# Kernel optimization log

Measured on AMD Instinct MI355X. Metric: run time of the kernel, lower is better.

The kernel has to match this reference:

```python
import jax, jax.numpy as jnp
import numpy as np

HEADS = 16

def split_heads(v, heads):
    # NOTE: faithful to the source: reshape [B,S,D] -> [B,S,h_dim,heads], then
    # transpose to [B,heads,S,h_dim]. This interleaves channels across heads
    # (different from the standard [B,S,heads,h_dim] split).
    B, S, D = v.shape
    hd = D // heads
    return v.reshape(B, S, hd, heads).transpose(0, 3, 1, 2)

def merge_heads(v):
    # [B,heads,S,h_dim] -> transpose [B,S,h_dim,heads] -> reshape [B,S,D]
    B, H, S, hd = v.shape
    return v.transpose(0, 2, 3, 1).reshape(B, S, H * hd)

def setup_inputs() -> dict:
    key = jax.random.key(0)
    ks = jax.random.split(key, 5)
    B, S, D = 2, 2048, 1024
    return {
        "x": jax.random.normal(ks[0], (B, S, D), dtype=jnp.float32),
        "qw": jax.random.normal(ks[1], (D, D), dtype=jnp.float32),
        "kw": jax.random.normal(ks[2], (D, D), dtype=jnp.float32),
        "vw": jax.random.normal(ks[3], (D, D), dtype=jnp.float32),
        "ow": jax.random.normal(ks[4], (D, D), dtype=jnp.float32),
    }

def reference(x, qw, kw, vw, ow):
    B, S, D = x.shape
    Q = split_heads(x @ qw, HEADS)  # [B,H,S,hd]
    K = split_heads(x @ kw, HEADS)
    V = split_heads(x @ vw, HEADS)
    # NOTE: scale is 1/sqrt(dim), NOT 1/sqrt(head_dim), as in the source.
    scale = 1.0 / jnp.sqrt(jnp.float32(D))
    score = jnp.einsum("bhqd,bhkd->bhqk", Q, K) * scale  # [B,H,S,S]
    causal = jnp.tril(jnp.ones((1, 1, S, S), dtype=score.dtype))
    score = score - 1e10 * (1.0 - causal)
    weights = jax.nn.softmax(score, axis=-1)
    attn = jnp.einsum("bhqk,bhkd->bhqd", weights, V)
    return merge_heads(attn) @ ow
```

## Files before the change

### kernel.cpp

```cpp
#include <hip/hip_runtime.h>


typedef __bf16 bf16x8 __attribute__((ext_vector_type(8)));
typedef __bf16 bf16x4 __attribute__((ext_vector_type(4)));
typedef float  f32x4  __attribute__((ext_vector_type(4)));

#define S_LEN  2048
#define DMODEL 1024
#define NHEADS 16
#define HDIM   64
#define LOG2E  1.44269504088896340736f

__device__ __forceinline__ void gll16(const __bf16* g, __bf16* l) {
    __builtin_amdgcn_global_load_lds(
        (const __attribute__((address_space(1))) unsigned int*)g,
        (__attribute__((address_space(3))) unsigned int*)l, 16, 0, 0);
}

__global__ __launch_bounds__(256) void conv_split(const float* __restrict__ x,
                                                  __bf16* __restrict__ hi,
                                                  __bf16* __restrict__ lo, int n4) {
    int i = blockIdx.x * 256 + threadIdx.x;
    if (i >= n4) return;
    float4 v = ((const float4*)x)[i];
    bf16x4 h, l;
#pragma unroll
    for (int c = 0; c < 4; c++) {
        float f = (&v.x)[c];
        __bf16 fh = (__bf16)f;
        h[c] = fh;
        l[c] = (__bf16)(f - (float)fh);
    }
    ((bf16x4*)hi)[i] = h;
    ((bf16x4*)lo)[i] = l;
}

__global__ __launch_bounds__(256) void transpose_all(
    const float* __restrict__ qw, const float* __restrict__ kw,
    const float* __restrict__ vw, const float* __restrict__ ow,
    __bf16* __restrict__ qwthi, __bf16* __restrict__ qwtlo,
    __bf16* __restrict__ kwthi, __bf16* __restrict__ kwtlo,
    __bf16* __restrict__ vwt,  __bf16* __restrict__ owt) {
    __shared__ float tile[32][33];
    int z = blockIdx.z;
    const float* w = (z == 0) ? qw : (z == 1) ? kw : (z == 2) ? vw : ow;
    int n0 = blockIdx.x * 32, k0 = blockIdx.y * 32;
    int tx = threadIdx.x & 31, ty = threadIdx.x >> 5;
#pragma unroll
    for (int i = 0; i < 32; i += 8)
        tile[ty + i][tx] = w[(k0 + ty + i) * DMODEL + n0 + tx];
    __syncthreads();
#pragma unroll
    for (int i = 0; i < 32; i += 8) {
        float f = tile[tx][ty + i];
        int k = k0 + tx, n = n0 + ty + i;
        if (z <= 1) {
            __bf16 fh = (__bf16)f;
            __bf16 fl = (__bf16)(f - (float)fh);
            int c = (n & 15) * 64 + (n >> 4);
            if (z == 0) { qwthi[c * DMODEL + k] = fh; qwtlo[c * DMODEL + k] = fl; }
            else        { kwthi[c * DMODEL + k] = fh; kwtlo[c * DMODEL + k] = fl; }
        } else if (z == 2) {
            vwt[n * DMODEL + k] = (__bf16)f;
        } else {
            int ck = (k & 15) * 64 + (k >> 4);
            owt[n * DMODEL + ck] = (__bf16)f;
        }
    }
}

__global__ __launch_bounds__(256) void qkv_gemm(
    const __bf16* __restrict__ xhi, const __bf16* __restrict__ xlo,
    const __bf16* __restrict__ qwthi, const __bf16* __restrict__ qwtlo,
    const __bf16* __restrict__ kwthi, const __bf16* __restrict__ kwtlo,
    const __bf16* __restrict__ vwt,
    __bf16* __restrict__ Qhi, __bf16* __restrict__ Qlo,
    __bf16* __restrict__ Khi, __bf16* __restrict__ Klo,
    __bf16* __restrict__ Vt) {
    __shared__ __bf16 Ash[128][32], Asl[128][32], Bsh[128][32], Bsl[128][32];
    int mode = blockIdx.z;
    int tid  = threadIdx.x;
    int wave = tid >> 6, lane = tid & 63;
    int quad = lane >> 4, l15 = lane & 15;
    int wm = (wave >> 1) * 64, wn = (wave & 1) * 64;
    int grow = lane >> 2, gcol = (lane & 3) * 8;
    const int K = DMODEL;

    if (mode < 2) {
        const __bf16* Bh = mode ? kwthi : qwthi;
        const __bf16* Bl = mode ? kwtlo : qwtlo;
        int m0 = blockIdx.y * 128, n0 = blockIdx.x * 128;
        f32x4 acc[4][4] = {};
        for (int k0 = 0; k0 < K; k0 += 32) {
            __syncthreads();
#pragma unroll
            for (int ps = 0; ps < 2; ps++) {
                int row = ps * 64 + wave * 16;
                gll16(&xhi[(m0 + row + grow) * K + k0 + gcol], &Ash[row][0]);
                gll16(&xlo[(m0 + row + grow) * K + k0 + gcol], &Asl[row][0]);
                gll16(&Bh [(n0 + row + grow) * K + k0 + gcol], &Bsh[row][0]);
                gll16(&Bl [(n0 + row + grow) * K + k0 + gcol], &Bsl[row][0]);
            }
            __syncthreads();
            bf16x8 ah[4], al[4], bh[4], bl[4];
#pragma unroll
            for (int mi = 0; mi < 4; mi++) {
                ah[mi] = *(const bf16x8*)&Ash[wm + mi * 16 + l15][quad * 8];
                al[mi] = *(const bf16x8*)&Asl[wm + mi * 16 + l15][quad * 8];
            }
#pragma unroll
            for (int ni = 0; ni < 4; ni++) {
                bh[ni] = *(const bf16x8*)&Bsh[wn + ni * 16 + l15][quad * 8];
                bl[ni] = *(const bf16x8*)&Bsl[wn + ni * 16 + l15][quad * 8];
            }
#pragma unroll
            for (int mi = 0; mi < 4; mi++)
#pragma unroll
                for (int ni = 0; ni < 4; ni++) {
                    acc[mi][ni] = __builtin_amdgcn_mfma_f32_16x16x32_bf16(ah[mi], bh[ni], acc[mi][ni], 0, 0, 0);
                    acc[mi][ni] = __builtin_amdgcn_mfma_f32_16x16x32_bf16(ah[mi], bl[ni], acc[mi][ni], 0, 0, 0);
                    acc[mi][ni] = __builtin_amdgcn_mfma_f32_16x16x32_bf16(al[mi], bh[ni], acc[mi][ni], 0, 0, 0);
                }
        }
        float oscale = mode ? 1.0f : 0.03125f * LOG2E;
        __bf16* Ohi = mode ? Khi : Qhi;
        __bf16* Olo = mode ? Klo : Qlo;
#pragma unroll
        for (int mi = 0; mi < 4; mi++)
#pragma unroll
            for (int ni = 0; ni < 4; ni++)
#pragma unroll
                for (int rg = 0; rg < 4; rg++) {
                    int m = m0 + wm + mi * 16 + quad * 4 + rg;
                    int n = n0 + wn + ni * 16 + l15;
                    float v = acc[mi][ni][rg] * oscale;
                    size_t idx = (size_t)m * DMODEL + n;
                    __bf16 vh = (__bf16)v;
                    Ohi[idx] = vh;
                    Olo[idx] = (__bf16)(v - (float)vh);
                }
    } else {
        int ch0 = blockIdx.x * 128, xm0 = blockIdx.y * 128;
        f32x4 acc[4][4] = {};
        for (int k0 = 0; k0 < K; k0 += 32) {
            __syncthreads();
#pragma unroll
            for (int ps = 0; ps < 2; ps++) {
                int row = ps * 64 + wave * 16;
                gll16(&vwt[(ch0 + row + grow) * K + k0 + gcol], &Ash[row][0]);
                gll16(&xhi[(xm0 + row + grow) * K + k0 + gcol], &Bsh[row][0]);
            }
            __syncthreads();
            bf16x8 af[4], bfr[4];
#pragma unroll
            for (int mi = 0; mi < 4; mi++)
                af[mi] = *(const bf16x8*)&Ash[wm + mi * 16 + l15][quad * 8];
#pragma unroll
            for (int ni = 0; ni < 4; ni++)
                bfr[ni] = *(const bf16x8*)&Bsh[wn + ni * 16 + l15][quad * 8];
#pragma unroll
            for (int mi = 0; mi < 4; mi++)
#pragma unroll
                for (int ni = 0; ni < 4; ni++)
                    acc[mi][ni] = __builtin_amdgcn_mfma_f32_16x16x32_bf16(
                        af[mi], bfr[ni], acc[mi][ni], 0, 0, 0);
        }
#pragma unroll
        for (int mi = 0; mi < 4; mi++)
#pragma unroll
            for (int ni = 0; ni < 4; ni++)
#pragma unroll
                for (int rg = 0; rg < 4; rg++) {
                    int ch = ch0 + wm + mi * 16 + quad * 4 + rg;
                    int xm = xm0 + wn + ni * 16 + l15;
                    int b = xm >> 11, s = xm & 2047;
                    int h = ch & 15,  d = ch >> 4;
                    Vt[((size_t)(b * NHEADS + h) * HDIM + d) * S_LEN + s] =
                        (__bf16)acc[mi][ni][rg];
                }
    }
}

__global__ __launch_bounds__(256) void out_gemm(const __bf16* __restrict__ A,
                                                const __bf16* __restrict__ Bt,
                                                float* __restrict__ out) {
    __shared__ __bf16 As[64][32];
    __shared__ __bf16 Bs[128][32];
    int tid  = threadIdx.x;
    int wave = tid >> 6, lane = tid & 63;
    int quad = lane >> 4, l15 = lane & 15;
    int m0 = blockIdx.y * 64, n0 = blockIdx.x * 128;
    int wm = (wave >> 1) * 32, wn = (wave & 1) * 64;
    int grow = lane >> 2, gcol = (lane & 3) * 8;
    const int K = DMODEL;
    f32x4 acc[2][4] = {};

    for (int k0 = 0; k0 < K; k0 += 32) {
        __syncthreads();
        gll16(&A[(m0 + wave * 16 + grow) * K + k0 + gcol], &As[wave * 16][0]);
#pragma unroll
        for (int ps = 0; ps < 2; ps++) {
            int row = ps * 64 + wave * 16;
            gll16(&Bt[(n0 + row + grow) * K + k0 + gcol], &Bs[row][0]);
        }
        __syncthreads();
        bf16x8 af[2], bfr[4];
#pragma unroll
        for (int mi = 0; mi < 2; mi++)
            af[mi] = *(const bf16x8*)&As[wm + mi * 16 + l15][quad * 8];
#pragma unroll
        for (int ni = 0; ni < 4; ni++)
            bfr[ni] = *(const bf16x8*)&Bs[wn + ni * 16 + l15][quad * 8];
#pragma unroll
        for (int mi = 0; mi < 2; mi++)
#pragma unroll
            for (int ni = 0; ni < 4; ni++)
                acc[mi][ni] = __builtin_amdgcn_mfma_f32_16x16x32_bf16(
                    af[mi], bfr[ni], acc[mi][ni], 0, 0, 0);
    }

#pragma unroll
    for (int mi = 0; mi < 2; mi++)
#pragma unroll
        for (int ni = 0; ni < 4; ni++)
#pragma unroll
            for (int rg = 0; rg < 4; rg++) {
                int m = m0 + wm + mi * 16 + quad * 4 + rg;
                int n = n0 + wn + ni * 16 + l15;
                out[(size_t)m * DMODEL + n] = acc[mi][ni][rg];
            }
}

__global__ __launch_bounds__(256, 4) void flash_attn(const __bf16* __restrict__ Qhi,
                                                     const __bf16* __restrict__ Qlo,
                                                     const __bf16* __restrict__ Khi,
                                                     const __bf16* __restrict__ Klo,
                                                     const __bf16* __restrict__ Vt,
                                                     __bf16* __restrict__ attn) {
    int id = blockIdx.x;
    int xcd = id & 7, which = id >> 3;
    int bh  = xcd + 8 * (which & 3);
    int p   = which >> 2;
    int b = bh >> 4, h = bh & 15;
    const __bf16* Qh_hi = Qhi + (size_t)b * S_LEN * DMODEL + h * HDIM;
    const __bf16* Qh_lo = Qlo + (size_t)b * S_LEN * DMODEL + h * HDIM;
    const __bf16* Kh_hi = Khi + (size_t)b * S_LEN * DMODEL + h * HDIM;
    const __bf16* Kh_lo = Klo + (size_t)b * S_LEN * DMODEL + h * HDIM;
    const __bf16* Vh    = Vt  + (size_t)bh * HDIM * S_LEN;

    int tid = threadIdx.x, wave = tid >> 6, lane = tid & 63;
    int quad = lane >> 4, l15 = lane & 15;
    int t1 = p, t2 = 31 - p;
    int n1 = t1 + 1;

    __shared__ __bf16 KhF[8 * 64 * 8];
    __shared__ __bf16 KlF[8 * 64 * 8];
    __shared__ __bf16 VF [8 * 64 * 8];
    __shared__ __bf16 Ps[4][16][72];

    int c1  = tid >> 6, key = tid & 63;
    int inner = (c1 * 16 + (key & 15)) * 8;
    int rK    = (key >> 4);
    int kdst0 = rK * 512 + inner, kdst1 = (4 + rK) * 512 + inner;
    const __bf16* vrow = Vh + (size_t)key * S_LEN;

    int q0w = t1 * 64 + wave * 16;
    bf16x8 aqh0 = *(const bf16x8*)&Qh_hi[(size_t)(q0w + l15) * DMODEL + quad * 8];
    bf16x8 aqh1 = *(const bf16x8*)&Qh_hi[(size_t)(q0w + l15) * DMODEL + 32 + quad * 8];
    bf16x8 aql0 = *(const bf16x8*)&Qh_lo[(size_t)(q0w + l15) * DMODEL + quad * 8];
    bf16x8 aql1 = *(const bf16x8*)&Qh_lo[(size_t)(q0w + l15) * DMODEL + 32 + quad * 8];

    bf16x8 ones;
#pragma unroll
    for (int j = 0; j < 8; j++) ones[j] = (__bf16)1.0f;

    uint4 pk0, pk1, pl0, pl1, pv0, pv1;
    {
        const __bf16* sk = Kh_hi + (size_t)key * DMODEL;
        const __bf16* sl = Kh_lo + (size_t)key * DMODEL;
        pk0 = *(const uint4*)(sk + c1 * 8); pk1 = *(const uint4*)(sk + c1 * 8 + 32);
        pl0 = *(const uint4*)(sl + c1 * 8); pl1 = *(const uint4*)(sl + c1 * 8 + 32);
        pv0 = *(const uint4*)(vrow + c1 * 8); pv1 = *(const uint4*)(vrow + c1 * 8 + 32);
    }

    float m[4] = {-3e38f, -3e38f, -3e38f, -3e38f};
    f32x4 o[4] = {};
    f32x4 ol = {};
    int qrb = q0w + quad * 4;

    for (int i = 0; i < 33; i++) {
        int kt   = (i < n1) ? i : i - n1;
        int key0 = kt * 64;
        bool diag = (i == n1 - 1) || (i == 32);

        __syncthreads();
        *(uint4*)&KhF[kdst0] = pk0;  *(uint4*)&KhF[kdst1] = pk1;
        *(uint4*)&KlF[kdst0] = pl0;  *(uint4*)&KlF[kdst1] = pl1;
        *(uint4*)&VF [kdst0] = pv0;  *(uint4*)&VF [kdst1] = pv1;
        __syncthreads();

        if (i + 1 < 33) {
            int ktn   = (i + 1 < n1) ? i + 1 : i + 1 - n1;
            int key0n = ktn * 64;
            const __bf16* sk = Kh_hi + (size_t)(key0n + key) * DMODEL;
            const __bf16* sl = Kh_lo + (size_t)(key0n + key) * DMODEL;
            pk0 = *(const uint4*)(sk + c1 * 8); pk1 = *(const uint4*)(sk + c1 * 8 + 32);
            pl0 = *(const uint4*)(sl + c1 * 8); pl1 = *(const uint4*)(sl + c1 * 8 + 32);
            pv0 = *(const uint4*)(vrow + key0n + c1 * 8);
            pv1 = *(const uint4*)(vrow + key0n + c1 * 8 + 32);
        }

        f32x4 sc[4] = {};
#pragma unroll
        for (int ni = 0; ni < 4; ni++) {
            bf16x8 kh0 = *(const bf16x8*)&KhF[(ni * 64 + lane) * 8];
            bf16x8 kh1 = *(const bf16x8*)&KhF[((4 + ni) * 64 + lane) * 8];
            bf16x8 kl0 = *(const bf16x8*)&KlF[(ni * 64 + lane) * 8];
            bf16x8 kl1 = *(const bf16x8*)&KlF[((4 + ni) * 64 + lane) * 8];
            sc[ni] = __builtin_amdgcn_mfma_f32_16x16x32_bf16(aqh0, kh0, sc[ni], 0, 0, 0);
            sc[ni] = __builtin_amdgcn_mfma_f32_16x16x32_bf16(aqh1, kh1, sc[ni], 0, 0, 0);
            sc[ni] = __builtin_amdgcn_mfma_f32_16x16x32_bf16(aqh0, kl0, sc[ni], 0, 0, 0);
            sc[ni] = __builtin_amdgcn_mfma_f32_16x16x32_bf16(aqh1, kl1, sc[ni], 0, 0, 0);
            sc[ni] = __builtin_amdgcn_mfma_f32_16x16x32_bf16(aql0, kh0, sc[ni], 0, 0, 0);
            sc[ni] = __builtin_amdgcn_mfma_f32_16x16x32_bf16(aql1, kh1, sc[ni], 0, 0, 0);
        }

        if (diag) {
#pragma unroll
            for (int ni = 0; ni < 4; ni++) {
                int keyi = key0 + ni * 16 + l15;
#pragma unroll
                for (int rg = 0; rg < 4; rg++)
                    if (keyi > qrb + rg) sc[ni][rg] = -1e30f;
            }
        }

#pragma unroll
        for (int rg = 0; rg < 4; rg++) {
            float mx = fmaxf(fmaxf(sc[0][rg], sc[1][rg]),
                             fmaxf(sc[2][rg], sc[3][rg]));
#pragma unroll
            for (int mm = 1; mm < 16; mm <<= 1)
                mx = fmaxf(mx, __shfl_xor(mx, mm, 64));
            float mnew  = fmaxf(m[rg], mx);
            float alpha = __builtin_amdgcn_exp2f(m[rg] - mnew);
            m[rg] = mnew;
#pragma unroll
            for (int ni = 0; ni < 4; ni++) {
                float px = __builtin_amdgcn_exp2f(sc[ni][rg] - mnew);
                Ps[wave][quad * 4 + rg][ni * 16 + l15] = (__bf16)px;
            }
            ol[rg] *= alpha;
#pragma unroll
            for (int ni = 0; ni < 4; ni++)
                o[ni][rg] *= alpha;
        }

#pragma unroll
        for (int step = 0; step < 2; step++) {
            bf16x8 ap = *(const bf16x8*)&Ps[wave][l15][step * 32 + quad * 8];
            ol = __builtin_amdgcn_mfma_f32_16x16x32_bf16(ap, ones, ol, 0, 0, 0);
#pragma unroll
            for (int ni = 0; ni < 4; ni++) {
                bf16x8 bv = *(const bf16x8*)&VF[((step * 4 + ni) * 64 + lane) * 8];
                o[ni] = __builtin_amdgcn_mfma_f32_16x16x32_bf16(ap, bv, o[ni], 0, 0, 0);
            }
        }

        if (diag) {
#pragma unroll
            for (int rg = 0; rg < 4; rg++) {
                float inv = 1.0f / ol[rg];
                int q = q0w + quad * 4 + rg;
#pragma unroll
                for (int ni = 0; ni < 4; ni++) {
                    attn[((size_t)b * S_LEN + q) * DMODEL + h * HDIM + ni * 16 + l15] =
                        (__bf16)(o[ni][rg] * inv);
                }
                m[rg] = -3e38f;
            }
#pragma unroll
            for (int ni = 0; ni < 4; ni++) o[ni] = (f32x4){0.f, 0.f, 0.f, 0.f};
            ol = (f32x4){0.f, 0.f, 0.f, 0.f};
            if (i == n1 - 1) {
                q0w = t2 * 64 + wave * 16;
                qrb = q0w + quad * 4;
                aqh0 = *(const bf16x8*)&Qh_hi[(size_t)(q0w + l15) * DMODEL + quad * 8];
                aqh1 = *(const bf16x8*)&Qh_hi[(size_t)(q0w + l15) * DMODEL + 32 + quad * 8];
                aql0 = *(const bf16x8*)&Qh_lo[(size_t)(q0w + l15) * DMODEL + quad * 8];
                aql1 = *(const bf16x8*)&Qh_lo[(size_t)(q0w + l15) * DMODEL + 32 + quad * 8];
            }
        }
    }
}

extern "C" void kernel_launch(void* const* d_in, const int* in_sizes, int n_in,
                              void* d_out, int out_size, void* d_ws, size_t ws_size,
                              hipStream_t stream) {
    const float* x  = (const float*)d_in[0];
    const float* qw = (const float*)d_in[1];
    const float* kw = (const float*)d_in[2];
    const float* vw = (const float*)d_in[3];
    const float* ow = (const float*)d_in[4];

    char* ws = (char*)d_ws;
    const size_t MB = 1024 * 1024;
    __bf16* xhi   = (__bf16*)(ws);
    __bf16* xlo   = (__bf16*)(ws + 8 * MB);
    __bf16* qwthi = (__bf16*)(ws + 16 * MB);
    __bf16* qwtlo = (__bf16*)(ws + 18 * MB);
    __bf16* kwthi = (__bf16*)(ws + 20 * MB);
    __bf16* kwtlo = (__bf16*)(ws + 22 * MB);
    __bf16* vwt   = (__bf16*)(ws + 24 * MB);
    __bf16* owt   = (__bf16*)(ws + 26 * MB);
    __bf16* Qhi_b = (__bf16*)(ws + 28 * MB);
    __bf16* Qlo_b = (__bf16*)(ws + 36 * MB);
    __bf16* Khi_b = (__bf16*)(ws + 44 * MB);
    __bf16* Klo_b = (__bf16*)(ws + 52 * MB);
    __bf16* Vtb   = (__bf16*)(ws + 60 * MB);
    __bf16* attnb = xlo;

    conv_split<<<4096, 256, 0, stream>>>(x, xhi, xlo, 4096 * 1024 / 4);
    transpose_all<<<dim3(32, 32, 4), 256, 0, stream>>>(
        qw, kw, vw, ow, qwthi, qwtlo, kwthi, kwtlo, vwt, owt);

    qkv_gemm<<<dim3(8, 32, 3), 256, 0, stream>>>(
        xhi, xlo, qwthi, qwtlo, kwthi, kwtlo, vwt,
        Qhi_b, Qlo_b, Khi_b, Klo_b, Vtb);

    flash_attn<<<512, 256, 0, stream>>>(Qhi_b, Qlo_b, Khi_b, Klo_b, Vtb, attnb);

    out_gemm<<<dim3(8, 64), 256, 0, stream>>>(attnb, owt, (float*)d_out);
}
```

Baseline: 254.5 us.

## Split paired causal query tiles into separate blocks, longest-first scheduling

The flash attention kernel no longer pairs query tile p with tile 31-p inside one block. It launches 1024 blocks, one per query tile, ordered so the longest tiles (most key tiles) are dispatched first and the hardware scheduler balances the rest. This doubles parallelism and simplifies the loop and epilogue, but each block now loads its Q and pays its own startup. The input split kernel is also rewritten to use scalar bit casts and ushort4 stores.

```diff
diff --git a/kernel.cpp b/kernel.cpp
--- a/kernel.cpp
+++ b/kernel.cpp
@@ -2,7 +2,6 @@
 
 
 typedef __bf16 bf16x8 __attribute__((ext_vector_type(8)));
-typedef __bf16 bf16x4 __attribute__((ext_vector_type(4)));
 typedef float  f32x4  __attribute__((ext_vector_type(4)));
 
 #define S_LEN  2048
@@ -23,16 +22,20 @@
     int i = blockIdx.x * 256 + threadIdx.x;
     if (i >= n4) return;
     float4 v = ((const float4*)x)[i];
-    bf16x4 h, l;
-#pragma unroll
-    for (int c = 0; c < 4; c++) {
-        float f = (&v.x)[c];
-        __bf16 fh = (__bf16)f;
-        h[c] = fh;
-        l[c] = (__bf16)(f - (float)fh);
-    }
-    ((bf16x4*)hi)[i] = h;
-    ((bf16x4*)lo)[i] = l;
+    __bf16 h0 = (__bf16)v.x, h1 = (__bf16)v.y, h2 = (__bf16)v.z, h3 = (__bf16)v.w;
+    bf16x8 dummy;
+    (void)dummy;
+    ushort4 hh, ll;
+    hh.x = __builtin_bit_cast(unsigned short, h0);
+    hh.y = __builtin_bit_cast(unsigned short, h1);
+    hh.z = __builtin_bit_cast(unsigned short, h2);
+    hh.w = __builtin_bit_cast(unsigned short, h3);
+    ll.x = __builtin_bit_cast(unsigned short, (__bf16)(v.x - (float)h0));
+    ll.y = __builtin_bit_cast(unsigned short, (__bf16)(v.y - (float)h1));
+    ll.z = __builtin_bit_cast(unsigned short, (__bf16)(v.z - (float)h2));
+    ll.w = __builtin_bit_cast(unsigned short, (__bf16)(v.w - (float)h3));
+    ((ushort4*)hi)[i] = hh;
+    ((ushort4*)lo)[i] = ll;
 }
 
 __global__ __launch_bounds__(256) void transpose_all(
@@ -237,10 +240,10 @@
                                                      const __bf16* __restrict__ Klo,
                                                      const __bf16* __restrict__ Vt,
                                                      __bf16* __restrict__ attn) {
-    int id = blockIdx.x;
-    int xcd = id & 7, which = id >> 3;
-    int bh  = xcd + 8 * (which & 3);
-    int p   = which >> 2;
+    int id  = blockIdx.x;
+    int xcd = id & 7, r = id >> 3;
+    int bh  = xcd + 8 * (r & 3);
+    int t   = 31 - (r >> 2);
     int b = bh >> 4, h = bh & 15;
     const __bf16* Qh_hi = Qhi + (size_t)b * S_LEN * DMODEL + h * HDIM;
     const __bf16* Qh_lo = Qlo + (size_t)b * S_LEN * DMODEL + h * HDIM;
@@ -250,8 +253,7 @@
 
     int tid = threadIdx.x, wave = tid >> 6, lane = tid & 63;
     int quad = lane >> 4, l15 = lane & 15;
-    int t1 = p, t2 = 31 - p;
-    int n1 = t1 + 1;
+    int iters = t + 1;
 
     __shared__ __bf16 KhF[8 * 64 * 8];
     __shared__ __bf16 KlF[8 * 64 * 8];
@@ -264,7 +266,7 @@
     int kdst0 = rK * 512 + inner, kdst1 = (4 + rK) * 512 + inner;
     const __bf16* vrow = Vh + (size_t)key * S_LEN;
 
-    int q0w = t1 * 64 + wave * 16;
+    int q0w = t * 64 + wave * 16;
     bf16x8 aqh0 = *(const bf16x8*)&Qh_hi[(size_t)(q0w + l15) * DMODEL + quad * 8];
     bf16x8 aqh1 = *(const bf16x8*)&Qh_hi[(size_t)(q0w + l15) * DMODEL + 32 + quad * 8];
     bf16x8 aql0 = *(const bf16x8*)&Qh_lo[(size_t)(q0w + l15) * DMODEL + quad * 8];
@@ -288,10 +290,9 @@
     f32x4 ol = {};
     int qrb = q0w + quad * 4;
 
-    for (int i = 0; i < 33; i++) {
-        int kt   = (i < n1) ? i : i - n1;
-        int key0 = kt * 64;
-        bool diag = (i == n1 - 1) || (i == 32);
+    for (int i = 0; i < iters; i++) {
+        int key0 = i * 64;
+        bool diag = (i == iters - 1);
 
         __syncthreads();
         *(uint4*)&KhF[kdst0] = pk0;  *(uint4*)&KhF[kdst1] = pk1;
@@ -299,9 +300,8 @@
         *(uint4*)&VF [kdst0] = pv0;  *(uint4*)&VF [kdst1] = pv1;
         __syncthreads();
 
-        if (i + 1 < 33) {
-            int ktn   = (i + 1 < n1) ? i + 1 : i + 1 - n1;
-            int key0n = ktn * 64;
+        if (i + 1 < iters) {
+            int key0n = (i + 1) * 64;
             const __bf16* sk = Kh_hi + (size_t)(key0n + key) * DMODEL;
             const __bf16* sl = Kh_lo + (size_t)(key0n + key) * DMODEL;
             pk0 = *(const uint4*)(sk + c1 * 8); pk1 = *(const uint4*)(sk + c1 * 8 + 32);
@@ -366,30 +366,16 @@
                 o[ni] = __builtin_amdgcn_mfma_f32_16x16x32_bf16(ap, bv, o[ni], 0, 0, 0);
             }
         }
-
-        if (diag) {
-#pragma unroll
-            for (int rg = 0; rg < 4; rg++) {
-                float inv = 1.0f / ol[rg];
-                int q = q0w + quad * 4 + rg;
-#pragma unroll
-                for (int ni = 0; ni < 4; ni++) {
-                    attn[((size_t)b * S_LEN + q) * DMODEL + h * HDIM + ni * 16 + l15] =
-                        (__bf16)(o[ni][rg] * inv);
-                }
-                m[rg] = -3e38f;
-            }
-#pragma unroll
-            for (int ni = 0; ni < 4; ni++) o[ni] = (f32x4){0.f, 0.f, 0.f, 0.f};
-            ol = (f32x4){0.f, 0.f, 0.f, 0.f};
-            if (i == n1 - 1) {
-                q0w = t2 * 64 + wave * 16;
-                qrb = q0w + quad * 4;
-                aqh0 = *(const bf16x8*)&Qh_hi[(size_t)(q0w + l15) * DMODEL + quad * 8];
-                aqh1 = *(const bf16x8*)&Qh_hi[(size_t)(q0w + l15) * DMODEL + 32 + quad * 8];
-                aql0 = *(const bf16x8*)&Qh_lo[(size_t)(q0w + l15) * DMODEL + quad * 8];
-                aql1 = *(const bf16x8*)&Qh_lo[(size_t)(q0w + l15) * DMODEL + 32 + quad * 8];
-            }
+    }
+
+#pragma unroll
+    for (int rg = 0; rg < 4; rg++) {
+        float inv = 1.0f / ol[rg];
+        int q = q0w + quad * 4 + rg;
+#pragma unroll
+        for (int ni = 0; ni < 4; ni++) {
+            attn[((size_t)b * S_LEN + q) * DMODEL + h * HDIM + ni * 16 + l15] =
+                (__bf16)(o[ni][rg] * inv);
         }
     }
 }
@@ -428,7 +414,7 @@
         xhi, xlo, qwthi, qwtlo, kwthi, kwtlo, vwt,
         Qhi_b, Qlo_b, Khi_b, Klo_b, Vtb);
 
-    flash_attn<<<512, 256, 0, stream>>>(Qhi_b, Qlo_b, Khi_b, Klo_b, Vtb, attnb);
+    flash_attn<<<1024, 256, 0, stream>>>(Qhi_b, Qlo_b, Khi_b, Klo_b, Vtb, attnb);
 
     out_gemm<<<dim3(8, 64), 256, 0, stream>>>(attnb, owt, (float*)d_out);
 }
```

After: 258.0 us. About the same (+1.4%).
